# Kernel tuning notes

Measured on AMD Instinct MI355X. Metric: run time of the kernel, lower is better.

Reference implementation:

```python
import jax, jax.numpy as jnp
import numpy as np

NUM_GRAPHS = 2048


def gcn_conv(x, W, b, edge, N):
    # PyG GCNConv: x' = D^{-1/2} (A + I) D^{-1/2} (x W) + b
    src, dst = edge[0], edge[1]
    loop = jnp.arange(N, dtype=src.dtype)
    src = jnp.concatenate([src, loop])
    dst = jnp.concatenate([dst, loop])
    h = x @ W  # [N, out]
    deg = jax.ops.segment_sum(jnp.ones(dst.shape, x.dtype), dst, num_segments=N)
    dinv = jnp.where(deg > 0, jax.lax.rsqrt(deg), 0.0)
    norm = dinv[src] * dinv[dst]  # [E+N]
    out = jax.ops.segment_sum(h[src] * norm[:, None], dst, num_segments=N)
    return out + b


def pool_max_mean(x, batch, G):
    mx = jax.ops.segment_max(x, batch, num_segments=G)
    mx = jnp.where(jnp.isfinite(mx), mx, 0.0)  # guard empty segments
    s = jax.ops.segment_sum(x, batch, num_segments=G)
    cnt = jax.ops.segment_sum(jnp.ones((x.shape[0],), x.dtype), batch, num_segments=G)
    mean = s / jnp.maximum(cnt, 1.0)[:, None]
    return mx, mean


def setup_inputs() -> dict:
    key = jax.random.key(0)
    ks = jax.random.split(key, 20)
    F, CE, SE, DD = 64, 64, 32, 128
    Nc, Ec, Ns, Es = 100000, 1250000, 100000, 1250000

    def glorot(k, shape):
        fan_in, fan_out = shape[0], shape[1]
        lim = np.sqrt(6.0 / (fan_in + fan_out)).astype(np.float32)
        return jax.random.uniform(k, shape, jnp.float32, -lim, lim)

    inp = {
        "c": jax.random.normal(ks[0], (Nc, F), jnp.float32),
        "c_edge": jax.random.randint(ks[1], (2, Ec), 0, Nc),
        "c_batch": jnp.sort(jax.random.randint(ks[2], (Nc,), 0, NUM_GRAPHS)),
        "s": jax.random.normal(ks[3], (Ns, F), jnp.float32),
        "s_edge": jax.random.randint(ks[4], (2, Es), 0, Ns),
        "s_batch": jnp.sort(jax.random.randint(ks[5], (Ns,), 0, NUM_GRAPHS)),
        "Wc0": glorot(ks[6], (F, CE)), "bc0": jnp.zeros((CE,), jnp.float32),
        "Wc1": glorot(ks[7], (CE, CE)), "bc1": jnp.zeros((CE,), jnp.float32),
        "Wc2": glorot(ks[8], (CE, CE)), "bc2": jnp.zeros((CE,), jnp.float32),
        "Ws0": glorot(ks[9], (F, SE)), "bs0": jnp.zeros((SE,), jnp.float32),
        "Ws1": glorot(ks[10], (SE, SE)), "bs1": jnp.zeros((SE,), jnp.float32),
        "Ws2": glorot(ks[11], (SE, SE)), "bs2": jnp.zeros((SE,), jnp.float32),
        "Wd": glorot(ks[12], ((CE + SE) * 2, DD)), "bd": jnp.zeros((DD,), jnp.float32),
        "Wo": glorot(ks[13], (DD, 1)), "bo": jnp.zeros((1,), jnp.float32),
    }
    return inp


def reference(c, c_edge, c_batch, s, s_edge, s_batch,
              Wc0, bc0, Wc1, bc1, Wc2, bc2,
              Ws0, bs0, Ws1, bs1, Ws2, bs2,
              Wd, bd, Wo, bo):
    Nc, Ns = c.shape[0], s.shape[0]
    cro = jax.nn.relu(gcn_conv(c, Wc0, bc0, c_edge, Nc))
    cro = jax.nn.relu(gcn_conv(cro, Wc1, bc1, c_edge, Nc))
    cro = jax.nn.relu(gcn_conv(cro, Wc2, bc2, c_edge, Nc))
    solv = jax.nn.relu(gcn_conv(s, Ws0, bs0, s_edge, Ns))
    solv = jax.nn.relu(gcn_conv(solv, Ws1, bs1, s_edge, Ns))
    solv = jax.nn.relu(gcn_conv(solv, Ws2, bs2, s_edge, Ns))
    c_mx, c_mean = pool_max_mean(cro, c_batch, NUM_GRAPHS)
    s_mx, s_mean = pool_max_mean(solv, s_batch, NUM_GRAPHS)
    embed = jnp.concatenate([c_mx, c_mean, s_mx, s_mean], axis=1)  # [G, 192]
    dense = jax.nn.relu(embed @ Wd + bd)
    out = dense @ Wo + bo  # [G, 1]
    return out, embed
```

## Files before the change

kernel.cpp:

```cpp
#include <hip/hip_runtime.h>
#include <hip/hip_fp16.h>
#include <math.h>


static inline int cdiv(int a, int b) { return (a + b - 1) / b; }

#define BUCKET_CAP 8192
#define P1_CHUNK   4096

typedef _Float16 v8h __attribute__((ext_vector_type(8)));
typedef float    v4f __attribute__((ext_vector_type(4)));

__global__ void zero_int(int* __restrict__ p, int n) {
    int i = blockIdx.x * blockDim.x + threadIdx.x;
    if (i < n) p[i] = 0;
}

__global__ __launch_bounds__(256) void p1_partition(const int* __restrict__ c_edge, int Ec,
                                                    const int* __restrict__ s_edge, int Es,
                                                    int Nc_pad, int Etot, int nbuck,
                                                    int* __restrict__ bucket_fill,
                                                    unsigned* __restrict__ pk) {
    __shared__ unsigned       wbuf[P1_CHUNK];
    __shared__ unsigned short bbuf[P1_CHUNK];
    __shared__ int            hist[512];
    int e0 = blockIdx.x * P1_CHUNK;
    int n  = Etot - e0;
    if (n > P1_CHUNK) n = P1_CHUNK;
    for (int i = threadIdx.x; i < nbuck; i += 256) hist[i] = 0;
    __syncthreads();
    for (int i = threadIdx.x; i < n; i += 256) {
        int e = e0 + i, src, g;
        if (e < Ec) { src = c_edge[e]; g = c_edge[Ec + e]; }
        else        { int e2 = e - Ec; src = s_edge[e2]; g = Nc_pad + s_edge[Es + e2]; }
        int b   = g >> 9;
        wbuf[i] = ((unsigned)(g & 511) << 17) | (unsigned)src;
        bbuf[i] = (unsigned short)b;
        atomicAdd(&hist[b], 1);
    }
    __syncthreads();
    for (int i = threadIdx.x; i < nbuck; i += 256) {
        int h = hist[i];
        hist[i] = h ? atomicAdd(&bucket_fill[i], h) : 0;
    }
    __syncthreads();
    for (int i = threadIdx.x; i < n; i += 256) {
        int b    = bbuf[i];
        int slot = atomicAdd(&hist[b], 1);
        if (slot < BUCKET_CAP) pk[(size_t)b * BUCKET_CAP + slot] = wbuf[i];
    }
}

__global__ __launch_bounds__(512) void p2_scanbuckets(const int* __restrict__ fill, int nbuck,
                                                      int* __restrict__ basearr,
                                                      int* __restrict__ off_all, int Ntot_pad, int Etot) {
    __shared__ int sh[512];
    int v = (threadIdx.x < nbuck) ? fill[threadIdx.x] : 0;
    sh[threadIdx.x] = v;
    __syncthreads();
    for (int ofs = 1; ofs < 512; ofs <<= 1) {
        int t = (threadIdx.x >= ofs) ? sh[threadIdx.x - ofs] : 0;
        __syncthreads();
        sh[threadIdx.x] += t;
        __syncthreads();
    }
    if (threadIdx.x < nbuck) basearr[threadIdx.x] = sh[threadIdx.x] - v;
    if (threadIdx.x == 0) off_all[Ntot_pad] = Etot;
}

__global__ __launch_bounds__(512) void p3_build(const unsigned* __restrict__ pk,
                                                const int* __restrict__ fillarr,
                                                const int* __restrict__ basearr,
                                                int* __restrict__ off_all,
                                                float* __restrict__ dinv,
                                                int* __restrict__ csr) {
    __shared__ int sh[512];
    int b    = blockIdx.x;
    int fill = fillarr[b];
    if (fill > BUCKET_CAP) fill = BUCKET_CAP;
    int base = basearr[b];
    const unsigned* reg = pk + (size_t)b * BUCKET_CAP;
    sh[threadIdx.x] = 0;
    __syncthreads();
    for (int i = threadIdx.x; i < fill; i += 512) atomicAdd(&sh[reg[i] >> 17], 1);
    __syncthreads();
    int cnt = sh[threadIdx.x];
    for (int ofs = 1; ofs < 512; ofs <<= 1) {
        int t = (threadIdx.x >= ofs) ? sh[threadIdx.x - ofs] : 0;
        __syncthreads();
        sh[threadIdx.x] += t;
        __syncthreads();
    }
    int excl = sh[threadIdx.x] - cnt;
    int node = b * 512 + threadIdx.x;
    off_all[node] = base + excl;
    dinv[node]    = rsqrtf((float)(cnt + 1));
    __syncthreads();
    sh[threadIdx.x] = excl;
    __syncthreads();
    for (int i = threadIdx.x; i < fill; i += 512) {
        unsigned w    = reg[i];
        int      slot = atomicAdd(&sh[w >> 17], 1);
        csr[base + slot] = (int)(w & 0x1FFFFu);
    }
}

template <int K, int M, typename TIN>
__device__ void gemm_mfma(int bid, const TIN* __restrict__ X, const float* __restrict__ W,
                          const float* __restrict__ dinv, __half* __restrict__ H, int N,
                          char* smem_) {
    constexpr int RB = 64;
    constexpr int KP = K + 8;
    constexpr int NT = M / 16;
    constexpr int KS = K / 32;
    _Float16* Xh = (_Float16*)smem_;
    _Float16* Wz = Xh + RB * KP;
    const int t    = threadIdx.x;
    const int row0 = bid * RB;

    constexpr int WENT = NT * KS * 64;
    for (int idx = t; idx < WENT; idx += 256) {
        int lane = idx & 63, rest = idx >> 6;
        int ks = rest % KS, ntl = rest / KS;
        int kbase = ks * 32 + (lane >> 4) * 8;
        int col   = ntl * 16 + (lane & 15);
        union { float4 f4; _Float16 h[8]; } u;
#pragma unroll
        for (int j = 0; j < 8; ++j) u.h[j] = (_Float16)W[(kbase + j) * M + col];
        *(float4*)(Wz + idx * 8) = u.f4;
    }
    if constexpr (sizeof(TIN) == 4) {
        constexpr int NI = RB * K / 4;
        for (int idx = t; idx < NI; idx += 256) {
            int row = idx / (K / 4), k4 = idx % (K / 4);
            int gr = row0 + row;
            float4 v = make_float4(0.f, 0.f, 0.f, 0.f);
            if (gr < N) v = *(const float4*)((const float*)X + (size_t)gr * K + k4 * 4);
            union { float2 f2; _Float16 h[4]; } u;
            u.h[0] = (_Float16)v.x; u.h[1] = (_Float16)v.y;
            u.h[2] = (_Float16)v.z; u.h[3] = (_Float16)v.w;
            *(float2*)(Xh + row * KP + k4 * 4) = u.f2;
        }
    } else {
        constexpr int NI = RB * K / 8;
        for (int idx = t; idx < NI; idx += 256) {
            int row = idx / (K / 8), k8 = idx % (K / 8);
            int gr = row0 + row;
            float4 v = make_float4(0.f, 0.f, 0.f, 0.f);
            if (gr < N) v = *(const float4*)((const __half*)X + (size_t)gr * K + k8 * 8);
            *(float4*)(Xh + row * KP + k8 * 8) = v;
        }
    }
    __syncthreads();

    const int wave = t >> 6, lane = t & 63;
    const int quad = lane >> 4, nl = lane & 15;
    const int rowA = wave * 16 + nl;

    v4f acc[NT];
#pragma unroll
    for (int i = 0; i < NT; ++i) acc[i] = (v4f){0.f, 0.f, 0.f, 0.f};

#pragma unroll
    for (int ks = 0; ks < KS; ++ks) {
        v8h a = *(const v8h*)(Xh + rowA * KP + ks * 32 + quad * 8);
#pragma unroll
        for (int ntl = 0; ntl < NT; ++ntl) {
            v8h b = *(const v8h*)(Wz + ((ntl * KS + ks) * 64 + lane) * 8);
            acc[ntl] = __builtin_amdgcn_mfma_f32_16x16x32_f16(a, b, acc[ntl], 0, 0, 0);
        }
    }

#pragma unroll
    for (int r = 0; r < 4; ++r) {
        int gr = row0 + wave * 16 + quad * 4 + r;
        if (gr < N) {
            float dv = dinv[gr];
#pragma unroll
            for (int ntl = 0; ntl < NT; ++ntl)
                H[(size_t)gr * M + ntl * 16 + nl] = __float2half(acc[ntl][r] * dv);
        }
    }
}

__device__ __forceinline__ float4 load4h(const float2* __restrict__ base, size_t idx) {
    float2 r = base[idx];
    union { float2 f2; __half2 h2[2]; } u;
    u.f2 = r;
    float2 a = __half22float2(u.h2[0]);
    float2 b = __half22float2(u.h2[1]);
    return make_float4(a.x, a.y, b.x, b.y);
}

__device__ __forceinline__ void load8h(const float4* __restrict__ base, size_t idx,
                                       float* __restrict__ o) {
    float4 r = base[idx];
    union { float4 f4; __half2 h2[4]; } u;
    u.f4 = r;
    float2 p0 = __half22float2(u.h2[0]);
    float2 p1 = __half22float2(u.h2[1]);
    float2 p2 = __half22float2(u.h2[2]);
    float2 p3 = __half22float2(u.h2[3]);
    o[0] = p0.x; o[1] = p0.y; o[2] = p1.x; o[3] = p1.y;
    o[4] = p2.x; o[5] = p2.y; o[6] = p3.x; o[7] = p3.y;
}

template <int MF>
__device__ void fused_agg_gemm(int bid, const __half* __restrict__ Hin,
                               const int* __restrict__ off_g, const int* __restrict__ csr,
                               const float* __restrict__ dinv_g, const float* __restrict__ b,
                               const float* __restrict__ W, __half* __restrict__ Hout,
                               int N, char* smem_) {
    constexpr int KP = MF + 8;
    constexpr int NT = MF / 16;
    constexpr int KS = MF / 32;
    _Float16* Xh = (_Float16*)smem_;
    _Float16* Wz = Xh + 64 * KP;
    const int t = threadIdx.x;

    constexpr int WENT = NT * KS * 64;
    for (int idx = t; idx < WENT; idx += 256) {
        int lane = idx & 63, rest = idx >> 6;
        int ks = rest % KS, ntl = rest / KS;
        int kbase = ks * 32 + (lane >> 4) * 8;
        int col   = ntl * 16 + (lane & 15);
        union { float4 f4; _Float16 h[8]; } u;
#pragma unroll
        for (int j = 0; j < 8; ++j) u.h[j] = (_Float16)W[(kbase + j) * MF + col];
        *(float4*)(Wz + idx * 8) = u.f4;
    }

    constexpr int L      = MF / 8;
    constexpr int NPW    = 64 / L;
    constexpr int PASSES = 64 / (4 * NPW);
    const int lane = t & 63, wave = t >> 6;
    const int fq = lane & (L - 1), sub = lane / L;
    const float4* H4 = (const float4*)Hin;
    const float4* b4 = (const float4*)b;
    float bb[8];
    {
        float4 b0 = b4[fq * 2], b1 = b4[fq * 2 + 1];
        bb[0] = b0.x; bb[1] = b0.y; bb[2] = b0.z; bb[3] = b0.w;
        bb[4] = b1.x; bb[5] = b1.y; bb[6] = b1.z; bb[7] = b1.w;
    }
#pragma unroll
    for (int pass = 0; pass < PASSES; ++pass) {
        int ln   = (pass * 4 + wave) * NPW + sub;
        int node = bid * 64 + ln;
        if (node < N) {
            int j0 = off_g[node], j1 = off_g[node + 1];
            float acc[8];
            load8h(H4, (size_t)node * L + fq, acc);
            int j = j0;
            for (; j + 8 <= j1; j += 8) {
                int s0 = csr[j],     s1 = csr[j + 1], s2 = csr[j + 2], s3 = csr[j + 3];
                int s4 = csr[j + 4], s5 = csr[j + 5], s6 = csr[j + 6], s7 = csr[j + 7];
                float a0[8], a1[8], a2[8], a3[8], a4[8], a5[8], a6[8], a7[8];
                load8h(H4, (size_t)s0 * L + fq, a0);
                load8h(H4, (size_t)s1 * L + fq, a1);
                load8h(H4, (size_t)s2 * L + fq, a2);
                load8h(H4, (size_t)s3 * L + fq, a3);
                load8h(H4, (size_t)s4 * L + fq, a4);
                load8h(H4, (size_t)s5 * L + fq, a5);
                load8h(H4, (size_t)s6 * L + fq, a6);
                load8h(H4, (size_t)s7 * L + fq, a7);
#pragma unroll
                for (int f = 0; f < 8; ++f) {
                    float g1 = ((a0[f] + a1[f]) + a2[f]) + a3[f];
                    float g2 = ((a4[f] + a5[f]) + a6[f]) + a7[f];
                    acc[f] += g1 + g2;
                }
            }
            for (; j + 4 <= j1; j += 4) {
                int s0 = csr[j], s1 = csr[j + 1], s2 = csr[j + 2], s3 = csr[j + 3];
                float a0[8], a1[8], a2[8], a3[8];
                load8h(H4, (size_t)s0 * L + fq, a0);
                load8h(H4, (size_t)s1 * L + fq, a1);
                load8h(H4, (size_t)s2 * L + fq, a2);
                load8h(H4, (size_t)s3 * L + fq, a3);
#pragma unroll
                for (int f = 0; f < 8; ++f)
                    acc[f] += ((a0[f] + a1[f]) + a2[f]) + a3[f];
            }
            for (; j < j1; ++j) {
                float a0[8];
                load8h(H4, (size_t)csr[j] * L + fq, a0);
#pragma unroll
                for (int f = 0; f < 8; ++f) acc[f] += a0[f];
            }
            float dv = dinv_g[node];
            union { float4 f4; __half2 h2[4]; } o;
#pragma unroll
            for (int p2 = 0; p2 < 4; ++p2) {
                float vx = dv * acc[2 * p2]     + bb[2 * p2];
                float vy = dv * acc[2 * p2 + 1] + bb[2 * p2 + 1];
                o.h2[p2] = __floats2half2_rn(vx > 0.f ? vx : 0.f, vy > 0.f ? vy : 0.f);
            }
            *(float4*)(Xh + ln * KP + fq * 8) = o.f4;
        } else {
            *(float4*)(Xh + ln * KP + fq * 8) = make_float4(0.f, 0.f, 0.f, 0.f);
        }
    }
    __syncthreads();

    const int quad = lane >> 4, nl = lane & 15;
    const int rowA = wave * 16 + nl;
    v4f acc2[NT];
#pragma unroll
    for (int i = 0; i < NT; ++i) acc2[i] = (v4f){0.f, 0.f, 0.f, 0.f};
#pragma unroll
    for (int ks = 0; ks < KS; ++ks) {
        v8h av = *(const v8h*)(Xh + rowA * KP + ks * 32 + quad * 8);
#pragma unroll
        for (int ntl = 0; ntl < NT; ++ntl) {
            v8h bv = *(const v8h*)(Wz + ((ntl * KS + ks) * 64 + lane) * 8);
            acc2[ntl] = __builtin_amdgcn_mfma_f32_16x16x32_f16(av, bv, acc2[ntl], 0, 0, 0);
        }
    }
#pragma unroll
    for (int r = 0; r < 4; ++r) {
        int gr = bid * 64 + wave * 16 + quad * 4 + r;
        if (gr < N) {
            float dv = dinv_g[gr];
#pragma unroll
            for (int ntl = 0; ntl < NT; ++ntl)
                Hout[(size_t)gr * MF + ntl * 16 + nl] = __float2half(acc2[ntl][r] * dv);
        }
    }
}

template <int M>
__device__ void agg_body(int bid, const __half* __restrict__ H,
                         const int* __restrict__ off_g,
                         const int* __restrict__ csr,
                         const float* __restrict__ dinv_g,
                         const float* __restrict__ b,
                         __half* __restrict__ out, int Nloc) {
    constexpr int L   = M / 4;
    constexpr int NPW = 64 / L;
    int lane = threadIdx.x & 63;
    int wave = threadIdx.x >> 6;
    int fq   = lane & (L - 1);
    int sub  = lane / L;
    int node = (bid * 4 + wave) * NPW + sub;
    if (node >= Nloc) return;
    const float2* H4 = (const float2*)H;
    int j0 = off_g[node], j1 = off_g[node + 1];
    float4 acc = load4h(H4, (size_t)node * L + fq);
    int j = j0;
    for (; j + 8 <= j1; j += 8) {
        int s0 = csr[j],     s1 = csr[j + 1], s2 = csr[j + 2], s3 = csr[j + 3];
        int s4 = csr[j + 4], s5 = csr[j + 5], s6 = csr[j + 6], s7 = csr[j + 7];
        float4 a0 = load4h(H4, (size_t)s0 * L + fq);
        float4 a1 = load4h(H4, (size_t)s1 * L + fq);
        float4 a2 = load4h(H4, (size_t)s2 * L + fq);
        float4 a3 = load4h(H4, (size_t)s3 * L + fq);
        float4 a4 = load4h(H4, (size_t)s4 * L + fq);
        float4 a5 = load4h(H4, (size_t)s5 * L + fq);
        float4 a6 = load4h(H4, (size_t)s6 * L + fq);
        float4 a7 = load4h(H4, (size_t)s7 * L + fq);
        acc.x += (a0.x + a1.x + a2.x + a3.x) + (a4.x + a5.x + a6.x + a7.x);
        acc.y += (a0.y + a1.y + a2.y + a3.y) + (a4.y + a5.y + a6.y + a7.y);
        acc.z += (a0.z + a1.z + a2.z + a3.z) + (a4.z + a5.z + a6.z + a7.z);
        acc.w += (a0.w + a1.w + a2.w + a3.w) + (a4.w + a5.w + a6.w + a7.w);
    }
    for (; j + 4 <= j1; j += 4) {
        int s0 = csr[j], s1 = csr[j + 1], s2 = csr[j + 2], s3 = csr[j + 3];
        float4 a0 = load4h(H4, (size_t)s0 * L + fq);
        float4 a1 = load4h(H4, (size_t)s1 * L + fq);
        float4 a2 = load4h(H4, (size_t)s2 * L + fq);
        float4 a3 = load4h(H4, (size_t)s3 * L + fq);
        acc.x += a0.x + a1.x + a2.x + a3.x;
        acc.y += a0.y + a1.y + a2.y + a3.y;
        acc.z += a0.z + a1.z + a2.z + a3.z;
        acc.w += a0.w + a1.w + a2.w + a3.w;
    }
    for (; j < j1; ++j) {
        float4 a = load4h(H4, (size_t)csr[j] * L + fq);
        acc.x += a.x; acc.y += a.y; acc.z += a.z; acc.w += a.w;
    }
    float  dv = dinv_g[node];
    float4 bb = ((const float4*)b)[fq];
    float  vx = dv * acc.x + bb.x;
    float  vy = dv * acc.y + bb.y;
    float  vz = dv * acc.z + bb.z;
    float  vw = dv * acc.w + bb.w;
    union { float2 f2; __half2 h2[2]; } o;
    o.h2[0] = __floats2half2_rn(vx > 0.f ? vx : 0.f, vy > 0.f ? vy : 0.f);
    o.h2[1] = __floats2half2_rn(vz > 0.f ? vz : 0.f, vw > 0.f ? vw : 0.f);
    ((float2*)out)[(size_t)node * L + fq] = o.f2;
}

__global__ __launch_bounds__(256) void gemmBoth0(const float* __restrict__ Xc, const float* __restrict__ Wc,
                                                 __half* __restrict__ cH, int Nc,
                                                 const float* __restrict__ Xs, const float* __restrict__ Ws,
                                                 __half* __restrict__ sH, int Ns,
                                                 const float* __restrict__ dinv_all, int Nc_pad, int nbC) {
    __shared__ __align__(16) char smem[17408];
    if (blockIdx.x < nbC) gemm_mfma<64, 64, float>(blockIdx.x, Xc, Wc, dinv_all, cH, Nc, smem);
    else                  gemm_mfma<64, 32, float>(blockIdx.x - nbC, Xs, Ws, dinv_all + Nc_pad, sH, Ns, smem);
}

__global__ __launch_bounds__(256) void fusedBoth(
        const __half* __restrict__ cHin, __half* __restrict__ cHout,
        const float* __restrict__ Wc, const float* __restrict__ bc,
        const __half* __restrict__ sHin, __half* __restrict__ sHout,
        const float* __restrict__ Ws, const float* __restrict__ bs,
        const int* __restrict__ off_all, const int* __restrict__ csr_all,
        const float* __restrict__ dinv_all,
        int Nc, int Ns, int Nc_pad, int nbC) {
    __shared__ __align__(16) char smem[17408];
    if (blockIdx.x < nbC)
        fused_agg_gemm<64>(blockIdx.x, cHin, off_all, csr_all, dinv_all, bc, Wc, cHout, Nc, smem);
    else
        fused_agg_gemm<32>(blockIdx.x - nbC, sHin, off_all + Nc_pad, csr_all,
                           dinv_all + Nc_pad, bs, Ws, sHout, Ns, smem);
}

__global__ __launch_bounds__(256) void aggBoth(const __half* __restrict__ cH, const __half* __restrict__ sH,
                                               const int* __restrict__ off_all, const int* __restrict__ csr_all,
                                               const float* __restrict__ dinv_all,
                                               const float* __restrict__ bc, const float* __restrict__ bs,
                                               __half* __restrict__ outc, __half* __restrict__ outs,
                                               int Nc, int Ns, int Nc_pad, int nbC) {
    if (blockIdx.x < nbC)
        agg_body<64>(blockIdx.x, cH, off_all, csr_all, dinv_all, bc, outc, Nc);
    else
        agg_body<32>(blockIdx.x - nbC, sH, off_all + Nc_pad, csr_all,
                     dinv_all + Nc_pad, bs, outs, Ns);
}

__device__ __forceinline__ int lbound(const int* __restrict__ a, int n, int key) {
    int lo = 0, hi = n;
    while (lo < hi) {
        int mid = (lo + hi) >> 1;
        if (a[mid] < key) lo = mid + 1; else hi = mid;
    }
    return lo;
}

__global__ __launch_bounds__(256) void poolDense(const __half* __restrict__ cX, const int* __restrict__ c_batch, int Nc,
                                                 const __half* __restrict__ sX, const int* __restrict__ s_batch, int Ns,
                                                 const float* __restrict__ Wd, const float* __restrict__ bd,
                                                 const float* __restrict__ Wo, const float* __restrict__ bo,
                                                 float* __restrict__ outv, float* __restrict__ embed) {
    __shared__ float e[192];
    __shared__ float red[512];
    __shared__ float rs[128];
    int g = blockIdx.x, t = threadIdx.x;
    int clo = lbound(c_batch, Nc, g), chi = lbound(c_batch, Nc, g + 1);
    {
        int f = t & 63, grp = t >> 6;
        float mx = 0.f, sm = 0.f;
        for (int i = clo + grp; i < chi; i += 4) {
            float v = __half2float(cX[(size_t)i * 64 + f]);
            mx = fmaxf(mx, v); sm += v;
        }
        red[grp * 64 + f]       = mx;
        red[256 + grp * 64 + f] = sm;
    }
    __syncthreads();
    if (t < 64) {
        float m = fmaxf(fmaxf(red[t], red[64 + t]), fmaxf(red[128 + t], red[192 + t]));
        float s = (red[256 + t] + red[320 + t]) + (red[384 + t] + red[448 + t]);
        int cn = chi - clo;
        e[t]      = m;
        e[64 + t] = s / (float)(cn > 0 ? cn : 1);
    }
    __syncthreads();
    int slo = lbound(s_batch, Ns, g), shi = lbound(s_batch, Ns, g + 1);
    {
        int f = t & 31, grp = t >> 5;
        float mx = 0.f, sm = 0.f;
        for (int i = slo + grp; i < shi; i += 8) {
            float v = __half2float(sX[(size_t)i * 32 + f]);
            mx = fmaxf(mx, v); sm += v;
        }
        red[grp * 32 + f]       = mx;
        red[256 + grp * 32 + f] = sm;
    }
    __syncthreads();
    if (t < 32) {
        float m = red[t];
        float s = red[256 + t];
#pragma unroll
        for (int grp = 1; grp < 8; ++grp) {
            m  = fmaxf(m, red[grp * 32 + t]);
            s += red[256 + grp * 32 + t];
        }
        int cn = shi - slo;
        e[128 + t] = m;
        e[160 + t] = s / (float)(cn > 0 ? cn : 1);
    }
    __syncthreads();
    if (t < 192) embed[(size_t)g * 192 + t] = e[t];
    if (t < 128) {
        float acc = bd[t];
        for (int k = 0; k < 192; ++k) acc += e[k] * Wd[k * 128 + t];
        float d = acc > 0.f ? acc : 0.f;
        rs[t] = d * Wo[t];
    }
    __syncthreads();
    for (int ofs = 64; ofs > 0; ofs >>= 1) {
        if (t < ofs) rs[t] += rs[t + ofs];
        __syncthreads();
    }
    if (t == 0) outv[g] = rs[0] + bo[0];
}


extern "C" void kernel_launch(void* const* d_in, const int* in_sizes, int n_in,
                              void* d_out, int out_size, void* d_ws, size_t ws_size,
                              hipStream_t stream) {
    const float* c       = (const float*)d_in[0];
    const int*   c_edge  = (const int*)d_in[1];
    const int*   c_batch = (const int*)d_in[2];
    const float* s       = (const float*)d_in[3];
    const int*   s_edge  = (const int*)d_in[4];
    const int*   s_batch = (const int*)d_in[5];
    const float* Wc0 = (const float*)d_in[6],  *bc0 = (const float*)d_in[7];
    const float* Wc1 = (const float*)d_in[8],  *bc1 = (const float*)d_in[9];
    const float* Wc2 = (const float*)d_in[10], *bc2 = (const float*)d_in[11];
    const float* Ws0 = (const float*)d_in[12], *bs0 = (const float*)d_in[13];
    const float* Ws1 = (const float*)d_in[14], *bs1 = (const float*)d_in[15];
    const float* Ws2 = (const float*)d_in[16], *bs2 = (const float*)d_in[17];
    const float* Wd  = (const float*)d_in[18], *bd  = (const float*)d_in[19];
    const float* Wo  = (const float*)d_in[20], *bo  = (const float*)d_in[21];

    const int Nc = in_sizes[0] / 64;
    const int Ec = in_sizes[1] / 2;
    const int Ns = in_sizes[3] / 64;
    const int Es = in_sizes[4] / 2;
    const int G  = out_size / 193;
    const int Nc_pad   = cdiv(Nc, 512) * 512;
    const int Ns_pad   = cdiv(Ns, 512) * 512;
    const int Ntot_pad = Nc_pad + Ns_pad;
    const int Etot     = Ec + Es;
    const int nbuck    = Ntot_pad >> 9;

    char* p = (char*)d_ws;
    auto  alloc = [&](size_t bytes) -> void* {
        void* r = (void*)p;
        p += (bytes + 255) & ~(size_t)255;
        return r;
    };
    int*      bucket_fill = (int*)alloc(512 * 4);
    int*      bucket_base = (int*)alloc(512 * 4);
    unsigned* pk          = (unsigned*)alloc((size_t)nbuck * BUCKET_CAP * 4);
    int*      off_all     = (int*)alloc(((size_t)Ntot_pad + 1) * 4);
    int*      csr_all     = (int*)alloc((size_t)Etot * 4);
    float*    dinv_all    = (float*)alloc((size_t)Ntot_pad * 4);
    __half*   bufC        = (__half*)alloc((size_t)Nc * 64 * 2);
    __half*   bufS        = (__half*)alloc((size_t)Ns * 32 * 2);
    __half*   cHa         = (__half*)alloc((size_t)Nc * 64 * 2);
    __half*   cHb         = (__half*)alloc((size_t)Nc * 64 * 2);
    __half*   sHa         = (__half*)alloc((size_t)Ns * 32 * 2);
    __half*   sHb         = (__half*)alloc((size_t)Ns * 32 * 2);

    float* outv  = (float*)d_out;
    float* embed = outv + G;

    const int nbGmC = cdiv(Nc, 64), nbGmS = cdiv(Ns, 64);
    const int nbFC  = cdiv(Nc, 64), nbFS  = cdiv(Ns, 64);
    const int nbAgC = Nc_pad / 16,  nbAgS = Ns_pad / 32;

    zero_int<<<cdiv(nbuck, 256), 256, 0, stream>>>(bucket_fill, nbuck);
    p1_partition<<<cdiv(Etot, P1_CHUNK), 256, 0, stream>>>(c_edge, Ec, s_edge, Es,
                                                           Nc_pad, Etot, nbuck, bucket_fill, pk);
    p2_scanbuckets<<<1, 512, 0, stream>>>(bucket_fill, nbuck, bucket_base, off_all, Ntot_pad, Etot);
    p3_build<<<nbuck, 512, 0, stream>>>(pk, bucket_fill, bucket_base,
                                        off_all, dinv_all, csr_all);

    gemmBoth0<<<nbGmC + nbGmS, 256, 0, stream>>>(c, Wc0, cHa, Nc, s, Ws0, sHa, Ns,
                                                 dinv_all, Nc_pad, nbGmC);

    fusedBoth<<<nbFC + nbFS, 256, 0, stream>>>(cHa, cHb, Wc1, bc0, sHa, sHb, Ws1, bs0,
                                               off_all, csr_all, dinv_all,
                                               Nc, Ns, Nc_pad, nbFC);
    fusedBoth<<<nbFC + nbFS, 256, 0, stream>>>(cHb, cHa, Wc2, bc1, sHb, sHa, Ws2, bs1,
                                               off_all, csr_all, dinv_all,
                                               Nc, Ns, Nc_pad, nbFC);

    aggBoth<<<nbAgC + nbAgS, 256, 0, stream>>>(cHa, sHa, off_all, csr_all, dinv_all,
                                               bc2, bs2, bufC, bufS, Nc, Ns, Nc_pad, nbAgC);

    poolDense<<<G, 256, 0, stream>>>(bufC, c_batch, Nc, bufS, s_batch, Ns,
                                     Wd, bd, Wo, bo, outv, embed);
}
```

Before: 355.5 us.

## Overlap first GEMM with edge partition and fuse last aggregation into pooling

```diff
diff --git a/kernel.cpp b/kernel.cpp
--- a/kernel.cpp
+++ b/kernel.cpp
@@ -16,15 +16,24 @@
     if (i < n) p[i] = 0;
 }
 
-__global__ __launch_bounds__(256) void p1_partition(const int* __restrict__ c_edge, int Ec,
-                                                    const int* __restrict__ s_edge, int Es,
-                                                    int Nc_pad, int Etot, int nbuck,
-                                                    int* __restrict__ bucket_fill,
-                                                    unsigned* __restrict__ pk) {
-    __shared__ unsigned       wbuf[P1_CHUNK];
-    __shared__ unsigned short bbuf[P1_CHUNK];
-    __shared__ int            hist[512];
-    int e0 = blockIdx.x * P1_CHUNK;
+__device__ __forceinline__ bool split_grid(int bid, int nMaj, int nMin, int& idx) {
+    int T  = nMaj + nMin;
+    int g0 = (int)(((long long)bid * nMin) / T);
+    int g1 = (int)(((long long)(bid + 1) * nMin) / T);
+    if (g1 > g0) { idx = g0; return true; }
+    idx = bid - g0;
+    return false;
+}
+
+__device__ void p1_body(int bid, const int* __restrict__ c_edge, int Ec,
+                        const int* __restrict__ s_edge, int Es,
+                        int Nc_pad, int Etot, int nbuck,
+                        int* __restrict__ bucket_fill,
+                        unsigned* __restrict__ pk, char* smem) {
+    unsigned*       wbuf = (unsigned*)smem;
+    unsigned short* bbuf = (unsigned short*)(smem + 16384);
+    int*            hist = (int*)(smem + 24576);
+    int e0 = bid * P1_CHUNK;
     int n  = Etot - e0;
     if (n > P1_CHUNK) n = P1_CHUNK;
     for (int i = threadIdx.x; i < nbuck; i += 256) hist[i] = 0;
@@ -105,7 +114,7 @@
     }
 }
 
-template <int K, int M, typename TIN>
+template <int K, int M, typename TIN, bool SCALE>
 __device__ void gemm_mfma(int bid, const TIN* __restrict__ X, const float* __restrict__ W,
                           const float* __restrict__ dinv, __half* __restrict__ H, int N,
                           char* smem_) {
@@ -175,7 +184,8 @@
     for (int r = 0; r < 4; ++r) {
         int gr = row0 + wave * 16 + quad * 4 + r;
         if (gr < N) {
-            float dv = dinv[gr];
+            float dv = 1.0f;
+            if constexpr (SCALE) dv = dinv[gr];
 #pragma unroll
             for (int ntl = 0; ntl < NT; ++ntl)
                 H[(size_t)gr * M + ntl * 16 + nl] = __float2half(acc[ntl][r] * dv);
@@ -183,29 +193,148 @@
     }
 }
 
-__device__ __forceinline__ float4 load4h(const float2* __restrict__ base, size_t idx) {
-    float2 r = base[idx];
-    union { float2 f2; __half2 h2[2]; } u;
-    u.f2 = r;
-    float2 a = __half22float2(u.h2[0]);
-    float2 b = __half22float2(u.h2[1]);
-    return make_float4(a.x, a.y, b.x, b.y);
-}
-
-__device__ __forceinline__ void load8h(const float4* __restrict__ base, size_t idx,
-                                       float* __restrict__ o) {
-    float4 r = base[idx];
+__device__ __forceinline__ void cvt8(float4 r, float* __restrict__ o) {
     union { float4 f4; __half2 h2[4]; } u;
     u.f4 = r;
-    float2 p0 = __half22float2(u.h2[0]);
-    float2 p1 = __half22float2(u.h2[1]);
-    float2 p2 = __half22float2(u.h2[2]);
-    float2 p3 = __half22float2(u.h2[3]);
-    o[0] = p0.x; o[1] = p0.y; o[2] = p1.x; o[3] = p1.y;
-    o[4] = p2.x; o[5] = p2.y; o[6] = p3.x; o[7] = p3.y;
-}
-
-template <int MF>
+    float2 p;
+    p = __half22float2(u.h2[0]); o[0] = p.x; o[1] = p.y;
+    p = __half22float2(u.h2[1]); o[2] = p.x; o[3] = p.y;
+    p = __half22float2(u.h2[2]); o[4] = p.x; o[5] = p.y;
+    p = __half22float2(u.h2[3]); o[6] = p.x; o[7] = p.y;
+}
+
+template <int L, bool SRCSCALE>
+__device__ void gather_row(const float4* __restrict__ H4, int node, int fq,
+                           const int* __restrict__ off_g, const int* __restrict__ csr,
+                           const float* __restrict__ dinv_g, float* __restrict__ acc) {
+    int j0 = off_g[node], j1 = off_g[node + 1];
+    {
+        float4 r = H4[(size_t)node * L + fq];
+        cvt8(r, acc);
+        if constexpr (SRCSCALE) {
+            float dvs = dinv_g[node];
+#pragma unroll
+            for (int f = 0; f < 8; ++f) acc[f] *= dvs;
+        }
+    }
+    float a[8];
+    int j = j0;
+    for (; j + 8 <= j1; j += 8) {
+        int s0 = csr[j],     s1 = csr[j + 1], s2 = csr[j + 2], s3 = csr[j + 3];
+        int s4 = csr[j + 4], s5 = csr[j + 5], s6 = csr[j + 6], s7 = csr[j + 7];
+        float4 r0 = H4[(size_t)s0 * L + fq];
+        float4 r1 = H4[(size_t)s1 * L + fq];
+        float4 r2 = H4[(size_t)s2 * L + fq];
+        float4 r3 = H4[(size_t)s3 * L + fq];
+        float4 r4 = H4[(size_t)s4 * L + fq];
+        float4 r5 = H4[(size_t)s5 * L + fq];
+        float4 r6 = H4[(size_t)s6 * L + fq];
+        float4 r7 = H4[(size_t)s7 * L + fq];
+        if constexpr (SRCSCALE) {
+            float d0 = dinv_g[s0], d1 = dinv_g[s1], d2 = dinv_g[s2], d3 = dinv_g[s3];
+            float d4 = dinv_g[s4], d5 = dinv_g[s5], d6 = dinv_g[s6], d7 = dinv_g[s7];
+            cvt8(r0, a);
+#pragma unroll
+            for (int f = 0; f < 8; ++f) acc[f] = fmaf(a[f], d0, acc[f]);
+            cvt8(r1, a);
+#pragma unroll
+            for (int f = 0; f < 8; ++f) acc[f] = fmaf(a[f], d1, acc[f]);
+            cvt8(r2, a);
+#pragma unroll
+            for (int f = 0; f < 8; ++f) acc[f] = fmaf(a[f], d2, acc[f]);
+            cvt8(r3, a);
+#pragma unroll
+            for (int f = 0; f < 8; ++f) acc[f] = fmaf(a[f], d3, acc[f]);
+            cvt8(r4, a);
+#pragma unroll
+            for (int f = 0; f < 8; ++f) acc[f] = fmaf(a[f], d4, acc[f]);
+            cvt8(r5, a);
+#pragma unroll
+            for (int f = 0; f < 8; ++f) acc[f] = fmaf(a[f], d5, acc[f]);
+            cvt8(r6, a);
+#pragma unroll
+            for (int f = 0; f < 8; ++f) acc[f] = fmaf(a[f], d6, acc[f]);
+            cvt8(r7, a);
+#pragma unroll
+            for (int f = 0; f < 8; ++f) acc[f] = fmaf(a[f], d7, acc[f]);
+        } else {
+            cvt8(r0, a);
+#pragma unroll
+            for (int f = 0; f < 8; ++f) acc[f] += a[f];
+            cvt8(r1, a);
+#pragma unroll
+            for (int f = 0; f < 8; ++f) acc[f] += a[f];
+            cvt8(r2, a);
+#pragma unroll
+            for (int f = 0; f < 8; ++f) acc[f] += a[f];
+            cvt8(r3, a);
+#pragma unroll
+            for (int f = 0; f < 8; ++f) acc[f] += a[f];
+            cvt8(r4, a);
+#pragma unroll
+            for (int f = 0; f < 8; ++f) acc[f] += a[f];
+            cvt8(r5, a);
+#pragma unroll
+            for (int f = 0; f < 8; ++f) acc[f] += a[f];
+            cvt8(r6, a);
+#pragma unroll
+            for (int f = 0; f < 8; ++f) acc[f] += a[f];
+            cvt8(r7, a);
+#pragma unroll
+            for (int f = 0; f < 8; ++f) acc[f] += a[f];
+        }
+    }
+    for (; j + 4 <= j1; j += 4) {
+        int s0 = csr[j], s1 = csr[j + 1], s2 = csr[j + 2], s3 = csr[j + 3];
+        float4 r0 = H4[(size_t)s0 * L + fq];
+        float4 r1 = H4[(size_t)s1 * L + fq];
+        float4 r2 = H4[(size_t)s2 * L + fq];
+        float4 r3 = H4[(size_t)s3 * L + fq];
+        if constexpr (SRCSCALE) {
+            float d0 = dinv_g[s0], d1 = dinv_g[s1], d2 = dinv_g[s2], d3 = dinv_g[s3];
+            cvt8(r0, a);
+#pragma unroll
+            for (int f = 0; f < 8; ++f) acc[f] = fmaf(a[f], d0, acc[f]);
+            cvt8(r1, a);
+#pragma unroll
+            for (int f = 0; f < 8; ++f) acc[f] = fmaf(a[f], d1, acc[f]);
+            cvt8(r2, a);
+#pragma unroll
+            for (int f = 0; f < 8; ++f) acc[f] = fmaf(a[f], d2, acc[f]);
+            cvt8(r3, a);
+#pragma unroll
+            for (int f = 0; f < 8; ++f) acc[f] = fmaf(a[f], d3, acc[f]);
+        } else {
+            cvt8(r0, a);
+#pragma unroll
+            for (int f = 0; f < 8; ++f) acc[f] += a[f];
+            cvt8(r1, a);
+#pragma unroll
+            for (int f = 0; f < 8; ++f) acc[f] += a[f];
+            cvt8(r2, a);
+#pragma unroll
+            for (int f = 0; f < 8; ++f) acc[f] += a[f];
+            cvt8(r3, a);
+#pragma unroll
+            for (int f = 0; f < 8; ++f) acc[f] += a[f];
+        }
+    }
+    for (; j < j1; ++j) {
+        int s0 = csr[j];
+        float4 r0 = H4[(size_t)s0 * L + fq];
+        cvt8(r0, a);
+        if constexpr (SRCSCALE) {
+            float d0 = dinv_g[s0];
+#pragma unroll
+            for (int f = 0; f < 8; ++f) acc[f] = fmaf(a[f], d0, acc[f]);
+        } else {
+#pragma unroll
+            for (int f = 0; f < 8; ++f) acc[f] += a[f];
+        }
+    }
+}
+
+template <int MF, bool SRCSCALE>
 __device__ void fused_agg_gemm(int bid, const __half* __restrict__ Hin,
                                const int* __restrict__ off_g, const int* __restrict__ csr,
                                const float* __restrict__ dinv_g, const float* __restrict__ b,
@@ -248,46 +377,8 @@
         int ln   = (pass * 4 + wave) * NPW + sub;
         int node = bid * 64 + ln;
         if (node < N) {
-            int j0 = off_g[node], j1 = off_g[node + 1];
             float acc[8];
-            load8h(H4, (size_t)node * L + fq, acc);
-            int j = j0;
-            for (; j + 8 <= j1; j += 8) {
-                int s0 = csr[j],     s1 = csr[j + 1], s2 = csr[j + 2], s3 = csr[j + 3];
-                int s4 = csr[j + 4], s5 = csr[j + 5], s6 = csr[j + 6], s7 = csr[j + 7];
-                float a0[8], a1[8], a2[8], a3[8], a4[8], a5[8], a6[8], a7[8];
-                load8h(H4, (size_t)s0 * L + fq, a0);
-                load8h(H4, (size_t)s1 * L + fq, a1);
-                load8h(H4, (size_t)s2 * L + fq, a2);
-                load8h(H4, (size_t)s3 * L + fq, a3);
-                load8h(H4, (size_t)s4 * L + fq, a4);
-                load8h(H4, (size_t)s5 * L + fq, a5);
-                load8h(H4, (size_t)s6 * L + fq, a6);
-                load8h(H4, (size_t)s7 * L + fq, a7);
-#pragma unroll
-                for (int f = 0; f < 8; ++f) {
-                    float g1 = ((a0[f] + a1[f]) + a2[f]) + a3[f];
-                    float g2 = ((a4[f] + a5[f]) + a6[f]) + a7[f];
-                    acc[f] += g1 + g2;
-                }
-            }
-            for (; j + 4 <= j1; j += 4) {
-                int s0 = csr[j], s1 = csr[j + 1], s2 = csr[j + 2], s3 = csr[j + 3];
-                float a0[8], a1[8], a2[8], a3[8];
-                load8h(H4, (size_t)s0 * L + fq, a0);
-                load8h(H4, (size_t)s1 * L + fq, a1);
-                load8h(H4, (size_t)s2 * L + fq, a2);
-                load8h(H4, (size_t)s3 * L + fq, a3);
-#pragma unroll
-                for (int f = 0; f < 8; ++f)
-                    acc[f] += ((a0[f] + a1[f]) + a2[f]) + a3[f];
-            }
-            for (; j < j1; ++j) {
-                float a0[8];
-                load8h(H4, (size_t)csr[j] * L + fq, a0);
-#pragma unroll
-                for (int f = 0; f < 8; ++f) acc[f] += a0[f];
-            }
+            gather_row<L, SRCSCALE>(H4, node, fq, off_g, csr, dinv_g, acc);
             float dv = dinv_g[node];
             union { float4 f4; __half2 h2[4]; } o;
 #pragma unroll
@@ -329,78 +420,87 @@
     }
 }
 
-template <int M>
-__device__ void agg_body(int bid, const __half* __restrict__ H,
-                         const int* __restrict__ off_g,
-                         const int* __restrict__ csr,
-                         const float* __restrict__ dinv_g,
-                         const float* __restrict__ b,
-                         __half* __restrict__ out, int Nloc) {
-    constexpr int L   = M / 4;
-    constexpr int NPW = 64 / L;
-    int lane = threadIdx.x & 63;
-    int wave = threadIdx.x >> 6;
-    int fq   = lane & (L - 1);
-    int sub  = lane / L;
-    int node = (bid * 4 + wave) * NPW + sub;
-    if (node >= Nloc) return;
-    const float2* H4 = (const float2*)H;
-    int j0 = off_g[node], j1 = off_g[node + 1];
-    float4 acc = load4h(H4, (size_t)node * L + fq);
-    int j = j0;
-    for (; j + 8 <= j1; j += 8) {
-        int s0 = csr[j],     s1 = csr[j + 1], s2 = csr[j + 2], s3 = csr[j + 3];
-        int s4 = csr[j + 4], s5 = csr[j + 5], s6 = csr[j + 6], s7 = csr[j + 7];
-        float4 a0 = load4h(H4, (size_t)s0 * L + fq);
-        float4 a1 = load4h(H4, (size_t)s1 * L + fq);
-        float4 a2 = load4h(H4, (size_t)s2 * L + fq);
-        float4 a3 = load4h(H4, (size_t)s3 * L + fq);
-        float4 a4 = load4h(H4, (size_t)s4 * L + fq);
-        float4 a5 = load4h(H4, (size_t)s5 * L + fq);
-        float4 a6 = load4h(H4, (size_t)s6 * L + fq);
-        float4 a7 = load4h(H4, (size_t)s7 * L + fq);
-        acc.x += (a0.x + a1.x + a2.x + a3.x) + (a4.x + a5.x + a6.x + a7.x);
-        acc.y += (a0.y + a1.y + a2.y + a3.y) + (a4.y + a5.y + a6.y + a7.y);
-        acc.z += (a0.z + a1.z + a2.z + a3.z) + (a4.z + a5.z + a6.z + a7.z);
-        acc.w += (a0.w + a1.w + a2.w + a3.w) + (a4.w + a5.w + a6.w + a7.w);
-    }
-    for (; j + 4 <= j1; j += 4) {
-        int s0 = csr[j], s1 = csr[j + 1], s2 = csr[j + 2], s3 = csr[j + 3];
-        float4 a0 = load4h(H4, (size_t)s0 * L + fq);
-        float4 a1 = load4h(H4, (size_t)s1 * L + fq);
-        float4 a2 = load4h(H4, (size_t)s2 * L + fq);
-        float4 a3 = load4h(H4, (size_t)s3 * L + fq);
-        acc.x += a0.x + a1.x + a2.x + a3.x;
-        acc.y += a0.y + a1.y + a2.y + a3.y;
-        acc.z += a0.z + a1.z + a2.z + a3.z;
-        acc.w += a0.w + a1.w + a2.w + a3.w;
-    }
-    for (; j < j1; ++j) {
-        float4 a = load4h(H4, (size_t)csr[j] * L + fq);
-        acc.x += a.x; acc.y += a.y; acc.z += a.z; acc.w += a.w;
-    }
-    float  dv = dinv_g[node];
-    float4 bb = ((const float4*)b)[fq];
-    float  vx = dv * acc.x + bb.x;
-    float  vy = dv * acc.y + bb.y;
-    float  vz = dv * acc.z + bb.z;
-    float  vw = dv * acc.w + bb.w;
-    union { float2 f2; __half2 h2[2]; } o;
-    o.h2[0] = __floats2half2_rn(vx > 0.f ? vx : 0.f, vy > 0.f ? vy : 0.f);
-    o.h2[1] = __floats2half2_rn(vz > 0.f ? vz : 0.f, vw > 0.f ? vw : 0.f);
-    ((float2*)out)[(size_t)node * L + fq] = o.f2;
-}
-
-__global__ __launch_bounds__(256) void gemmBoth0(const float* __restrict__ Xc, const float* __restrict__ Wc,
-                                                 __half* __restrict__ cH, int Nc,
-                                                 const float* __restrict__ Xs, const float* __restrict__ Ws,
-                                                 __half* __restrict__ sH, int Ns,
-                                                 const float* __restrict__ dinv_all, int Nc_pad, int nbC) {
-    __shared__ __align__(16) char smem[17408];
-    if (blockIdx.x < nbC) gemm_mfma<64, 64, float>(blockIdx.x, Xc, Wc, dinv_all, cH, Nc, smem);
-    else                  gemm_mfma<64, 32, float>(blockIdx.x - nbC, Xs, Ws, dinv_all + Nc_pad, sH, Ns, smem);
-}
-
+__device__ __forceinline__ int lbound(const int* __restrict__ a, int n, int key) {
+    int lo = 0, hi = n;
+    while (lo < hi) {
+        int mid = (lo + hi) >> 1;
+        if (a[mid] < key) lo = mid + 1; else hi = mid;
+    }
+    return lo;
+}
+
+template <int MF>
+__device__ void agg_pool(int g, const __half* __restrict__ Hin,
+                         const int* __restrict__ off_g, const int* __restrict__ csr,
+                         const float* __restrict__ dinv_g, const float* __restrict__ b,
+                         const int* __restrict__ batch, int Nbatch,
+                         float* __restrict__ embed, int eofs, float* __restrict__ smem) {
+    constexpr int L     = MF / 8;
+    constexpr int SLOTS = 256 / L;
+    const int t = threadIdx.x, fq = t & (L - 1), slot = t / L;
+    const int lo = lbound(batch, Nbatch, g), hi = lbound(batch, Nbatch, g + 1);
+    const float4* H4 = (const float4*)Hin;
+    const float4* b4 = (const float4*)b;
+    float bb[8];
+    {
+        float4 b0 = b4[fq * 2], b1 = b4[fq * 2 + 1];
+        bb[0] = b0.x; bb[1] = b0.y; bb[2] = b0.z; bb[3] = b0.w;
+        bb[4] = b1.x; bb[5] = b1.y; bb[6] = b1.z; bb[7] = b1.w;
+    }
+    float pmx[8], psm[8];
+#pragma unroll
+    for (int f = 0; f < 8; ++f) { pmx[f] = 0.f; psm[f] = 0.f; }
+    for (int node = lo + slot; node < hi; node += SLOTS) {
+        float acc[8];
+        gather_row<L, false>(H4, node, fq, off_g, csr, dinv_g, acc);
+        float dv = dinv_g[node];
+#pragma unroll
+        for (int f = 0; f < 8; ++f) {
+            float v = fmaf(dv, acc[f], bb[f]);
+            v = v > 0.f ? v : 0.f;
+            pmx[f] = fmaxf(pmx[f], v);
+            psm[f] += v;
+        }
+    }
+    float* lmx = smem;
+    float* lsm = smem + SLOTS * MF;
+    *(float4*)(lmx + slot * MF + fq * 8)     = *(float4*)(pmx);
+    *(float4*)(lmx + slot * MF + fq * 8 + 4) = *(float4*)(pmx + 4);
+    *(float4*)(lsm + slot * MF + fq * 8)     = *(float4*)(psm);
+    *(float4*)(lsm + slot * MF + fq * 8 + 4) = *(float4*)(psm + 4);
+    __syncthreads();
+    if (t < MF) {
+        float m = lmx[t], s = lsm[t];
+#pragma unroll 4
+        for (int sl = 1; sl < SLOTS; ++sl) {
+            m = fmaxf(m, lmx[sl * MF + t]);
+            s += lsm[sl * MF + t];
+        }
+        int cn = hi - lo;
+        embed[(size_t)g * 192 + eofs + t]      = m;
+        embed[(size_t)g * 192 + eofs + MF + t] = s / (float)(cn > 0 ? cn : 1);
+    }
+}
+
+__global__ __launch_bounds__(256) void p1_gemm0(
+        const int* __restrict__ c_edge, int Ec, const int* __restrict__ s_edge, int Es,
+        int Nc_pad, int Etot, int nbuck,
+        int* __restrict__ bucket_fill, unsigned* __restrict__ pk,
+        const float* __restrict__ Xc, const float* __restrict__ Wc0, __half* __restrict__ cH, int Nc,
+        const float* __restrict__ Xs, const float* __restrict__ Ws0, __half* __restrict__ sH, int Ns,
+        int nP1, int nGemC, int nGemS) {
+    __shared__ __align__(16) char smem[26624];
+    int idx;
+    if (split_grid(blockIdx.x, nGemC + nGemS, nP1, idx)) {
+        p1_body(idx, c_edge, Ec, s_edge, Es, Nc_pad, Etot, nbuck, bucket_fill, pk, smem);
+    } else if (idx < nGemC) {
+        gemm_mfma<64, 64, float, false>(idx, Xc, Wc0, (const float*)nullptr, cH, Nc, smem);
+    } else {
+        gemm_mfma<64, 32, float, false>(idx - nGemC, Xs, Ws0, (const float*)nullptr, sH, Ns, smem);
+    }
+}
+
+template <bool SRCSCALE>
 __global__ __launch_bounds__(256) void fusedBoth(
         const __half* __restrict__ cHin, __half* __restrict__ cHout,
         const float* __restrict__ Wc, const float* __restrict__ bc,
@@ -411,101 +511,50 @@
         int Nc, int Ns, int Nc_pad, int nbC) {
     __shared__ __align__(16) char smem[17408];
     if (blockIdx.x < nbC)
-        fused_agg_gemm<64>(blockIdx.x, cHin, off_all, csr_all, dinv_all, bc, Wc, cHout, Nc, smem);
+        fused_agg_gemm<64, SRCSCALE>(blockIdx.x, cHin, off_all, csr_all, dinv_all, bc, Wc, cHout, Nc, smem);
     else
-        fused_agg_gemm<32>(blockIdx.x - nbC, sHin, off_all + Nc_pad, csr_all,
-                           dinv_all + Nc_pad, bs, Ws, sHout, Ns, smem);
-}
-
-__global__ __launch_bounds__(256) void aggBoth(const __half* __restrict__ cH, const __half* __restrict__ sH,
-                                               const int* __restrict__ off_all, const int* __restrict__ csr_all,
-                                               const float* __restrict__ dinv_all,
-                                               const float* __restrict__ bc, const float* __restrict__ bs,
-                                               __half* __restrict__ outc, __half* __restrict__ outs,
-                                               int Nc, int Ns, int Nc_pad, int nbC) {
-    if (blockIdx.x < nbC)
-        agg_body<64>(blockIdx.x, cH, off_all, csr_all, dinv_all, bc, outc, Nc);
+        fused_agg_gemm<32, SRCSCALE>(blockIdx.x - nbC, sHin, off_all + Nc_pad, csr_all,
+                                     dinv_all + Nc_pad, bs, Ws, sHout, Ns, smem);
+}
+
+__global__ __launch_bounds__(256) void aggPoolBoth(
+        const __half* __restrict__ cH, const __half* __restrict__ sH,
+        const int* __restrict__ off_all, const int* __restrict__ csr_all,
+        const float* __restrict__ dinv_all,
+        const float* __restrict__ bc, const float* __restrict__ bs,
+        const int* __restrict__ c_batch, const int* __restrict__ s_batch,
+        int Nc, int Ns, int Nc_pad,
+        float* __restrict__ embed) {
+    __shared__ float smem[4096];
+    int bid = blockIdx.x;
+    int g   = bid >> 1;
+    if ((bid & 1) == 0)
+        agg_pool<64>(g, cH, off_all, csr_all, dinv_all, bc, c_batch, Nc, embed, 0, smem);
     else
-        agg_body<32>(blockIdx.x - nbC, sH, off_all + Nc_pad, csr_all,
-                     dinv_all + Nc_pad, bs, outs, Ns);
-}
-
-__device__ __forceinline__ int lbound(const int* __restrict__ a, int n, int key) {
-    int lo = 0, hi = n;
-    while (lo < hi) {
-        int mid = (lo + hi) >> 1;
-        if (a[mid] < key) lo = mid + 1; else hi = mid;
-    }
-    return lo;
-}
-
-__global__ __launch_bounds__(256) void poolDense(const __half* __restrict__ cX, const int* __restrict__ c_batch, int Nc,
-                                                 const __half* __restrict__ sX, const int* __restrict__ s_batch, int Ns,
-                                                 const float* __restrict__ Wd, const float* __restrict__ bd,
-                                                 const float* __restrict__ Wo, const float* __restrict__ bo,
-                                                 float* __restrict__ outv, float* __restrict__ embed) {
+        agg_pool<32>(g, sH, off_all + Nc_pad, csr_all, dinv_all + Nc_pad, bs,
+                     s_batch, Ns, embed, 128, smem);
+}
+
+__global__ __launch_bounds__(128) void denseHead(
+        const float* __restrict__ embed,
+        const float* __restrict__ Wd, const float* __restrict__ bd,
+        const float* __restrict__ Wo, const float* __restrict__ bo,
+        float* __restrict__ outv) {
     __shared__ float e[192];
-    __shared__ float red[512];
-    __shared__ float rs[128];
+    __shared__ float red[128];
     int g = blockIdx.x, t = threadIdx.x;
-    int clo = lbound(c_batch, Nc, g), chi = lbound(c_batch, Nc, g + 1);
-    {
-        int f = t & 63, grp = t >> 6;
-        float mx = 0.f, sm = 0.f;
-        for (int i = clo + grp; i < chi; i += 4) {
-            float v = __half2float(cX[(size_t)i * 64 + f]);
-            mx = fmaxf(mx, v); sm += v;
-        }
-        red[grp * 64 + f]       = mx;
-        red[256 + grp * 64 + f] = sm;
-    }
-    __syncthreads();
-    if (t < 64) {
-        float m = fmaxf(fmaxf(red[t], red[64 + t]), fmaxf(red[128 + t], red[192 + t]));
-        float s = (red[256 + t] + red[320 + t]) + (red[384 + t] + red[448 + t]);
-        int cn = chi - clo;
-        e[t]      = m;
-        e[64 + t] = s / (float)(cn > 0 ? cn : 1);
-    }
-    __syncthreads();
-    int slo = lbound(s_batch, Ns, g), shi = lbound(s_batch, Ns, g + 1);
-    {
-        int f = t & 31, grp = t >> 5;
-        float mx = 0.f, sm = 0.f;
-        for (int i = slo + grp; i < shi; i += 8) {
-            float v = __half2float(sX[(size_t)i * 32 + f]);
-            mx = fmaxf(mx, v); sm += v;
-        }
-        red[grp * 32 + f]       = mx;
-        red[256 + grp * 32 + f] = sm;
-    }
-    __syncthreads();
-    if (t < 32) {
-        float m = red[t];
-        float s = red[256 + t];
-#pragma unroll
-        for (int grp = 1; grp < 8; ++grp) {
-            m  = fmaxf(m, red[grp * 32 + t]);
-            s += red[256 + grp * 32 + t];
-        }
-        int cn = shi - slo;
-        e[128 + t] = m;
-        e[160 + t] = s / (float)(cn > 0 ? cn : 1);
-    }
-    __syncthreads();
-    if (t < 192) embed[(size_t)g * 192 + t] = e[t];
-    if (t < 128) {
-        float acc = bd[t];
-        for (int k = 0; k < 192; ++k) acc += e[k] * Wd[k * 128 + t];
-        float d = acc > 0.f ? acc : 0.f;
-        rs[t] = d * Wo[t];
-    }
+    for (int k = t; k < 192; k += 128) e[k] = embed[(size_t)g * 192 + k];
+    __syncthreads();
+    float acc = bd[t];
+    for (int k = 0; k < 192; ++k) acc += e[k] * Wd[k * 128 + t];
+    float d = acc > 0.f ? acc : 0.f;
+    red[t]  = d * Wo[t];
     __syncthreads();
     for (int ofs = 64; ofs > 0; ofs >>= 1) {
-        if (t < ofs) rs[t] += rs[t + ofs];
+        if (t < ofs) red[t] += red[t + ofs];
         __syncthreads();
     }
-    if (t == 0) outv[g] = rs[0] + bo[0];
+    if (t == 0) outv[g] = red[0] + bo[0];
 }
 
 
@@ -550,8 +599,6 @@
     int*      off_all     = (int*)alloc(((size_t)Ntot_pad + 1) * 4);
     int*      csr_all     = (int*)alloc((size_t)Etot * 4);
     float*    dinv_all    = (float*)alloc((size_t)Ntot_pad * 4);
-    __half*   bufC        = (__half*)alloc((size_t)Nc * 64 * 2);
-    __half*   bufS        = (__half*)alloc((size_t)Ns * 32 * 2);
     __half*   cHa         = (__half*)alloc((size_t)Nc * 64 * 2);
     __half*   cHb         = (__half*)alloc((size_t)Nc * 64 * 2);
     __half*   sHa         = (__half*)alloc((size_t)Ns * 32 * 2);
@@ -562,28 +609,28 @@
 
     const int nbGmC = cdiv(Nc, 64), nbGmS = cdiv(Ns, 64);
     const int nbFC  = cdiv(Nc, 64), nbFS  = cdiv(Ns, 64);
-    const int nbAgC = Nc_pad / 16,  nbAgS = Ns_pad / 32;
+    const int nP1   = cdiv(Etot, P1_CHUNK);
 
     zero_int<<<cdiv(nbuck, 256), 256, 0, stream>>>(bucket_fill, nbuck);
-    p1_partition<<<cdiv(Etot, P1_CHUNK), 256, 0, stream>>>(c_edge, Ec, s_edge, Es,
-                                                           Nc_pad, Etot, nbuck, bucket_fill, pk);
+
+    p1_gemm0<<<nP1 + nbGmC + nbGmS, 256, 0, stream>>>(
+        c_edge, Ec, s_edge, Es, Nc_pad, Etot, nbuck, bucket_fill, pk,
+        c, Wc0, cHa, Nc, s, Ws0, sHa, Ns, nP1, nbGmC, nbGmS);
+
     p2_scanbuckets<<<1, 512, 0, stream>>>(bucket_fill, nbuck, bucket_base, off_all, Ntot_pad, Etot);
     p3_build<<<nbuck, 512, 0, stream>>>(pk, bucket_fill, bucket_base,
                                         off_all, dinv_all, csr_all);
 
-    gemmBoth0<<<nbGmC + nbGmS, 256, 0, stream>>>(c, Wc0, cHa, Nc, s, Ws0, sHa, Ns,
-                                                 dinv_all, Nc_pad, nbGmC);
-
-    fusedBoth<<<nbFC + nbFS, 256, 0, stream>>>(cHa, cHb, Wc1, bc0, sHa, sHb, Ws1, bs0,
-                                               off_all, csr_all, dinv_all,
-                                               Nc, Ns, Nc_pad, nbFC);
-    fusedBoth<<<nbFC + nbFS, 256, 0, stream>>>(cHb, cHa, Wc2, bc1, sHb, sHa, Ws2, bs1,
-                                               off_all, csr_all, dinv_all,
-                                               Nc, Ns, Nc_pad, nbFC);
-
-    aggBoth<<<nbAgC + nbAgS, 256, 0, stream>>>(cHa, sHa, off_all, csr_all, dinv_all,
-                                               bc2, bs2, bufC, bufS, Nc, Ns, Nc_pad, nbAgC);
-
-    poolDense<<<G, 256, 0, stream>>>(bufC, c_batch, Nc, bufS, s_batch, Ns,
-                                     Wd, bd, Wo, bo, outv, embed);
-}
+    fusedBoth<true><<<nbFC + nbFS, 256, 0, stream>>>(
+        cHa, cHb, Wc1, bc0, sHa, sHb, Ws1, bs0,
+        off_all, csr_all, dinv_all, Nc, Ns, Nc_pad, nbFC);
+    fusedBoth<false><<<nbFC + nbFS, 256, 0, stream>>>(
+        cHb, cHa, Wc2, bc1, sHb, sHa, Ws2, bs1,
+        off_all, csr_all, dinv_all, Nc, Ns, Nc_pad, nbFC);
+
+    aggPoolBoth<<<2 * G, 256, 0, stream>>>(
+        cHa, sHa, off_all, csr_all, dinv_all, bc2, bs2,
+        c_batch, s_batch, Nc, Ns, Nc_pad, embed);
+
+    denseHead<<<G, 128, 0, stream>>>(embed, Wd, bd, Wo, bo, outv);
+}
```

Result: slower. 374.5 us (+5.3%).
